# Optimization experiments

Hardware: AMD Instinct MI355X
Metric: run time of the kernel (lower is better)

## Reference

```python
import jax, jax.numpy as jnp
import numpy as np

C = 256
G = 32  # GroupNorm groups
EPS = 1e-6


def setup_inputs() -> dict:
    key = jax.random.key(0)
    ks = jax.random.split(key, 11)
    B, H, W = 4, 64, 64
    scale = 0.02
    return {
        "x": jax.random.normal(ks[0], (B, C, H, W), dtype=jnp.float32),
        "gn_scale": jnp.ones((C,), jnp.float32),
        "gn_bias": jnp.zeros((C,), jnp.float32),
        "wq": jax.random.normal(ks[1], (C, C), jnp.float32) * scale,
        "bq": jnp.zeros((C,), jnp.float32),
        "wk": jax.random.normal(ks[2], (C, C), jnp.float32) * scale,
        "bk": jnp.zeros((C,), jnp.float32),
        "wv": jax.random.normal(ks[3], (C, C), jnp.float32) * scale,
        "bv": jnp.zeros((C,), jnp.float32),
        "wp": jax.random.normal(ks[4], (C, C), jnp.float32) * scale,
        "bp": jnp.zeros((C,), jnp.float32),
    }


def _group_norm(x, scale, bias):
    b, c, h, w = x.shape
    xr = x.reshape(b, G, c // G, h, w)
    mu = jnp.mean(xr, axis=(2, 3, 4), keepdims=True)
    var = jnp.var(xr, axis=(2, 3, 4), keepdims=True)
    xn = ((xr - mu) * jax.lax.rsqrt(var + EPS)).reshape(b, c, h, w)
    return xn * scale[None, :, None, None] + bias[None, :, None, None]


def _conv1x1(x, w, bch):
    # 1x1 conv == channel-mixing matmul; w is (out_ch, in_ch)
    return jnp.einsum('bchw,dc->bdhw', x, w) + bch[None, :, None, None]


def reference(x, gn_scale, gn_bias, wq, bq, wk, bk, wv, bv, wp, bp):
    b, c, h, w = x.shape
    hn = _group_norm(x, gn_scale, gn_bias)
    q = _conv1x1(hn, wq, bq).reshape(b, c, h * w)  # (b,c,N)
    k = _conv1x1(hn, wk, bk).reshape(b, c, h * w)
    v = _conv1x1(hn, wv, bv).reshape(b, c, h * w)
    # attn[b,i,j] = softmax_j( q_i . k_j / sqrt(c) )
    attn = jax.nn.softmax(jnp.einsum('bci,bcj->bij', q, k) * (c ** -0.5), axis=-1)
    A = jnp.einsum('bcj,bij->bci', v, attn).reshape(b, c, h, w)
    return x + _conv1x1(A, wp, bp)
```

## Files before the change

### kernel.cpp

```cpp
#include <hip/hip_runtime.h>
#include <stdint.h>

#define Bn 4
#define Cn 256
#define Gn 32
#define Nn 4096
#define CGn 8

typedef unsigned short u16;
typedef __attribute__((ext_vector_type(8))) short short8;
typedef __attribute__((ext_vector_type(4))) short short4v;
typedef __attribute__((ext_vector_type(4))) float f32x4;
typedef __attribute__((ext_vector_type(16))) float f32x16;

__device__ __forceinline__ u16 f2bf(float x) {
  uint32_t u = __float_as_uint(x);
  u += 0x7fffu + ((u >> 16) & 1u);
  return (u16)(u >> 16);
}
__device__ __forceinline__ float b2f(u16 v) {
  return __uint_as_float(((uint32_t)v) << 16);
}

__device__ __forceinline__ void gl_lds16(const void* g, void* l) {
  __builtin_amdgcn_global_load_lds(
      (__attribute__((address_space(1))) void*)(uintptr_t)g,
      (__attribute__((address_space(3))) void*)(uintptr_t)l, 16, 0, 0);
}

__device__ __forceinline__ int sw512(int row, int cb) { return row * 512 + ((cb ^ (row & 7)) * 16); }

__global__ void k_cs(const float* __restrict__ wq, const float* __restrict__ wk,
                     const float* __restrict__ wv, const float* __restrict__ wp,
                     const float* __restrict__ bq, const float* __restrict__ bk,
                     const float* __restrict__ bv, const float* __restrict__ x,
                     u16* __restrict__ wqkv, u16* __restrict__ wpb,
                     float* __restrict__ bqkv, float* __restrict__ stats) {
  if (blockIdx.x < 256) {
    const float s = 0.09016844005556021f;
    int i = blockIdx.x * 256 + threadIdx.x;
    wqkv[i]          = f2bf(wq[i] * s);
    wqkv[i + 65536]  = f2bf(wk[i]);
    wqkv[i + 131072] = f2bf(wv[i]);
    wpb[i]           = f2bf(wp[i]);
    if (i < 256) { bqkv[i] = bq[i] * s; bqkv[i + 256] = bk[i]; bqkv[i + 512] = bv[i]; }
  } else {
    int blk = blockIdx.x - 256;
    int grp = blk >> 2, part = blk & 3;
    const float4* base = (const float4*)(x + (size_t)grp * (CGn * Nn) + part * 8192);
    float s = 0.f, s2 = 0.f;
    for (int i = threadIdx.x; i < 2048; i += 256) {
      float4 v = base[i];
      s  += v.x + v.y + v.z + v.w;
      s2 += v.x * v.x + v.y * v.y + v.z * v.z + v.w * v.w;
    }
#pragma unroll
    for (int m = 1; m < 64; m <<= 1) { s += __shfl_xor(s, m, 64); s2 += __shfl_xor(s2, m, 64); }
    __shared__ float ps[4], ps2[4];
    int w = threadIdx.x >> 6;
    if ((threadIdx.x & 63) == 0) { ps[w] = s; ps2[w] = s2; }
    __syncthreads();
    if (threadIdx.x == 0) {
      stats[grp * 8 + part * 2]     = ps[0] + ps[1] + ps[2] + ps[3];
      stats[grp * 8 + part * 2 + 1] = ps2[0] + ps2[1] + ps2[2] + ps2[3];
    }
  }
}

__global__ void k_apply(const float* __restrict__ x, const float* __restrict__ stats,
                        const float* __restrict__ gsc, const float* __restrict__ gbi,
                        u16* __restrict__ hnT) {
  __shared__ __align__(16) char smem[32768];
  __shared__ float smu[Gn], srs[Gn];
  int n0 = blockIdx.x * 64;
  int b = blockIdx.y;
  int tid = threadIdx.x;
  if (tid < Gn) {
    float S = 0.f, S2 = 0.f;
#pragma unroll
    for (int p = 0; p < 4; ++p) {
      S  += stats[(b * Gn + tid) * 8 + p * 2];
      S2 += stats[(b * Gn + tid) * 8 + p * 2 + 1];
    }
    const float inv = 1.f / (CGn * Nn);
    float mu = S * inv;
    float var = S2 * inv - mu * mu;
    smu[tid] = mu;
    srs[tid] = rsqrtf(var + 1e-6f);
  }
  __syncthreads();
  int nl = (tid & 15) * 4;
  int cbase = tid >> 4;
  for (int pass = 0; pass < 16; ++pass) {
    int c = pass * 16 + cbase;
    float4 v = *(const float4*)(x + (size_t)b * Cn * Nn + (size_t)c * Nn + n0 + nl);
    int g = c >> 3;
    float sc = gsc[c] * srs[g];
    float bi = gbi[c] - smu[g] * sc;
    float vals[4] = {v.x, v.y, v.z, v.w};
#pragma unroll
    for (int i = 0; i < 4; ++i) {
      int row = nl + i;
      int off = row * 512 + ((((c >> 3) + row) & 31) * 16) + (c & 7) * 2;
      *(u16*)(smem + off) = f2bf(vals[i] * sc + bi);
    }
  }
  __syncthreads();
#pragma unroll
  for (int p = 0; p < 8; ++p) {
    int idx = p * 256 + tid;
    int row = idx >> 5, pc = idx & 31;
    int gc = (pc - row) & 31;
    short8 v8 = *(const short8*)(smem + row * 512 + pc * 16);
    *(short8*)(hnT + ((size_t)b * Nn + n0 + row) * Cn + gc * 8) = v8;
  }
}

__global__ __launch_bounds__(256, 2)
void k_qkv(const u16* __restrict__ wqkv, const float* __restrict__ bqkv,
           const u16* __restrict__ hnT, u16* __restrict__ qT, u16* __restrict__ kT,
           u16* __restrict__ vv) {
  __shared__ __align__(16) char smem[65536];
  int tid = threadIdx.x, lane = tid & 63, w = tid >> 6, quad = lane >> 4, low = lane & 15;
  int n0 = blockIdx.x * 64, d0 = blockIdx.y * 64, b = blockIdx.z;
  {
    int r0 = w * 16;
#pragma unroll
    for (int s = 0; s < 8; ++s) {
      int rs = r0 + s * 2;
      int r = rs + (lane >> 5);
      int cb = (lane & 31) ^ (r & 7);
      gl_lds16(wqkv + (size_t)(d0 + r) * Cn + cb * 8, smem + rs * 512);
      gl_lds16(hnT + ((size_t)b * Nn + n0 + r) * Cn + cb * 8, smem + 32768 + rs * 512);
    }
  }
  asm volatile("s_waitcnt vmcnt(0)" ::: "memory");
  __syncthreads();
  f32x4 acc[4] = {{0.f,0.f,0.f,0.f},{0.f,0.f,0.f,0.f},{0.f,0.f,0.f,0.f},{0.f,0.f,0.f,0.f}};
#pragma unroll
  for (int kk = 0; kk < 8; ++kk) {
    short8 af = *(const short8*)(smem + sw512(w * 16 + low, kk * 4 + quad));
#pragma unroll
    for (int t = 0; t < 4; ++t) {
      short8 bf = *(const short8*)(smem + 32768 + sw512(t * 16 + low, kk * 4 + quad));
      acc[t] = __builtin_amdgcn_mfma_f32_16x16x32_bf16(af, bf, acc[t], 0, 0, 0);
    }
  }
  int which = d0 >> 8;
  float bias[4];
#pragma unroll
  for (int r = 0; r < 4; ++r) bias[r] = bqkv[d0 + w * 16 + quad * 4 + r];
  __syncthreads();
  if (which == 2) {
#pragma unroll
    for (int t = 0; t < 4; ++t)
#pragma unroll
      for (int r = 0; r < 4; ++r) {
        int row = w * 16 + quad * 4 + r;
        int col = t * 16 + low;
        int off = row * 128 + ((((col >> 3) ^ ((row >> 1) & 7)) & 7) * 16) + (col & 7) * 2;
        *(u16*)(smem + off) = f2bf(acc[t][r] + bias[r]);
      }
  } else {
#pragma unroll
    for (int t = 0; t < 4; ++t)
#pragma unroll
      for (int r = 0; r < 4; ++r) {
        int row = t * 16 + low;
        int col = w * 16 + quad * 4 + r;
        int off = row * 128 + ((((col >> 3) ^ ((row >> 1) & 7)) & 7) * 16) + (col & 7) * 2;
        *(u16*)(smem + off) = f2bf(acc[t][r] + bias[r]);
      }
  }
  __syncthreads();
  int dl0 = d0 & 255;
#pragma unroll
  for (int p = 0; p < 2; ++p) {
    int idx = p * 256 + tid;
    int row = idx >> 3, pc = idx & 7;
    int cb = pc ^ ((row >> 1) & 7);
    short8 v8 = *(const short8*)(smem + row * 128 + pc * 16);
    if (which == 2)
      *(short8*)(vv + (size_t)b * Cn * Nn + (size_t)(dl0 + row) * Nn + n0 + cb * 8) = v8;
    else {
      u16* dst = (which == 0 ? qT : kT) + (size_t)b * Nn * Cn;
      *(short8*)(dst + (size_t)(n0 + row) * Cn + dl0 + cb * 8) = v8;
    }
  }
}

__device__ __forceinline__ void flash_stage(char* smem, int bsel, const u16* kTb,
                                            const u16* vb, int j0, int w, int lo,
                                            int kr, int vr, int vp) {
  char* ksb = smem + bsel * 32768;
  char* vsb = ksb + 16384;
#pragma unroll
  for (int s = 0; s < 4; ++s) {
    int j = kr + s * 2;
    int gc = (lo - j) & 31;
    gl_lds16(kTb + (size_t)(j0 + j) * Cn + gc * 8, ksb + (w * 8 + s * 2) * 512);
  }
#pragma unroll
  for (int s = 0; s < 4; ++s) {
    int c = vr + s * 16;
    int gc = (vp - c) & 3;
    gl_lds16(vb + (size_t)c * Nn + j0 + gc * 8, vsb + (w * 64 + s * 16) * 64);
  }
}

__global__ __launch_bounds__(256, 2)
void k_flash(const u16* __restrict__ qT, const u16* __restrict__ kT,
             const u16* __restrict__ vv, u16* __restrict__ Op0,
             u16* __restrict__ Op1, u16* __restrict__ Op2, u16* __restrict__ Op3,
             float* __restrict__ lrow) {
  __shared__ __align__(16) char smem[65536];
  const int tid = threadIdx.x, lane = tid & 63, w = tid >> 6;
  const int lo = lane & 31, hi = lane >> 5;
  const int i0 = blockIdx.x * 128;
  const int b = blockIdx.y, jh = blockIdx.z;
  const u16* qTb = qT + (size_t)b * Nn * Cn;
  const u16* kTb = kT + (size_t)b * Nn * Cn;
  const u16* vb  = vv + (size_t)b * Cn * Nn;
  const int u7 = lo + hi;
  const int kr = w * 8 + hi;
  const int vr = w * 64 + (lane >> 2);
  const int vp = lane & 3;

  flash_stage(smem, 0, kTb, vb, jh * 1024, w, lo, kr, vr, vp);

  short8 qf[16];
  {
    const u16* qrow = qTb + (size_t)(i0 + w * 32 + lo) * Cn + hi * 8;
#pragma unroll
    for (int ks = 0; ks < 16; ++ks) qf[ks] = *(const short8*)(qrow + ks * 16);
  }
  f32x16 Oa[8];
#pragma unroll
  for (int ct = 0; ct < 8; ++ct)
#pragma unroll
    for (int e = 0; e < 16; ++e) Oa[ct][e] = 0.f;
  float l_ = 0.f;

  for (int jt = 0; jt < 32; ++jt) {
    if (jt < 31) {
      flash_stage(smem, (jt + 1) & 1, kTb, vb, jh * 1024 + (jt + 1) * 32, w, lo, kr, vr, vp);
      asm volatile("s_waitcnt vmcnt(8)" ::: "memory");
    } else {
      asm volatile("s_waitcnt vmcnt(0)" ::: "memory");
    }
    asm volatile("s_barrier" ::: "memory");
    const char* ksb = smem + (jt & 1) * 32768;
    const char* vsb = ksb + 16384;

    f32x16 S0;
#pragma unroll
    for (int e = 0; e < 16; ++e) S0[e] = 0.f;
#pragma unroll
    for (int ks = 0; ks < 16; ++ks) {
      int ch = (ks * 2 + u7) & 31;
      short8 a0 = *(const short8*)(ksb + lo * 512 + ch * 16);
      S0 = __builtin_amdgcn_mfma_f32_32x32x16_bf16(a0, qf[ks], S0, 0, 0, 0);
    }
    uint32_t Pp[8];
#pragma unroll
    for (int g = 0; g < 8; ++g) {
      float p0 = __builtin_amdgcn_exp2f(S0[2 * g]);
      float p1 = __builtin_amdgcn_exp2f(S0[2 * g + 1]);
      l_ += p0 + p1;
      Pp[g] = ((uint32_t)f2bf(p1) << 16) | f2bf(p0);
    }
#pragma unroll
    for (int kst = 0; kst < 2; ++kst) {
      uint32_t a0 = Pp[4 * kst], a1 = Pp[4 * kst + 1];
      uint32_t b0 = Pp[4 * kst + 2], b1 = Pp[4 * kst + 3];
      uint32_t s0 = hi ? a0 : b0, s1 = hi ? a1 : b1;
      uint32_t r0 = (uint32_t)__shfl_xor((int)s0, 32, 64);
      uint32_t r1 = (uint32_t)__shfl_xor((int)s1, 32, 64);
      union { uint32_t u[4]; short8 s8; } pu;
      pu.u[0] = hi ? r0 : a0;
      pu.u[1] = hi ? r1 : a1;
      pu.u[2] = hi ? b0 : r0;
      pu.u[3] = hi ? b1 : r1;
      int ch = (kst * 2 + u7) & 3;
#pragma unroll
      for (int ct = 0; ct < 8; ++ct) {
        short8 vf = *(const short8*)(vsb + (ct * 32 + lo) * 64 + ch * 16);
        Oa[ct] = __builtin_amdgcn_mfma_f32_32x32x16_bf16(vf, pu.s8, Oa[ct], 0, 0, 0);
      }
    }
    asm volatile("s_barrier" ::: "memory");
  }

  l_ += __shfl_xor(l_, 32, 64);
  if (hi == 0)
    lrow[(size_t)jh * (Bn * Nn) + (size_t)b * Nn + i0 + w * 32 + lo] = l_;
  float invl = __builtin_amdgcn_rcpf(l_);
  __syncthreads();
#pragma unroll
  for (int ct = 0; ct < 8; ++ct)
#pragma unroll
    for (int g = 0; g < 4; ++g) {
      short4v pk;
#pragma unroll
      for (int r = 0; r < 4; ++r) pk[r] = (short)f2bf(Oa[ct][g * 4 + r] * invl);
      int chv = (ct * 4 + g + lo) & 31;
      *(short4v*)(smem + w * 16384 + lo * 512 + chv * 16 + hi * 8) = pk;
    }
  __syncthreads();
  u16* Opj = (jh == 0) ? Op0 : (jh == 1) ? Op1 : (jh == 2) ? Op2 : Op3;
  u16* Ob = Opj + ((size_t)b * Nn + i0 + w * 32) * (size_t)Cn;
#pragma unroll
  for (int s = 0; s < 16; ++s) {
    int rr = s * 2 + hi;
    short8 v8 = *(const short8*)(smem + w * 16384 + rr * 512 + lo * 16);
    int gc = (lo - rr) & 31;
    *(short8*)(Ob + (size_t)rr * Cn + gc * 8) = v8;
  }
}

__global__ __launch_bounds__(256, 2)
void k_proj(const u16* __restrict__ wpb, const float* __restrict__ bp,
            const u16* __restrict__ O0, const u16* __restrict__ O1,
            const u16* __restrict__ O2, const u16* __restrict__ O3,
            const float* __restrict__ lrow, const float* __restrict__ x,
            float* __restrict__ out) {
  __shared__ __align__(16) char smem[65536];
  int tid = threadIdx.x, lane = tid & 63, w = tid >> 6, quad = lane >> 4, low = lane & 15;
  int n0 = blockIdx.x * 64, d0 = blockIdx.y * 64, b = blockIdx.z;
  {
    int r0 = w * 16;
#pragma unroll
    for (int s = 0; s < 8; ++s) {
      int rs = r0 + s * 2;
      int r = rs + (lane >> 5);
      int cb = (lane & 31) ^ (r & 7);
      gl_lds16(wpb + (size_t)(d0 + r) * Cn + cb * 8, smem + rs * 512);
    }
#pragma unroll
    for (int s = 0; s < 8; ++s) {
      int rs = r0 + s * 2 + (lane >> 5);
      int cb = lane & 31;
      size_t rg = (size_t)b * Nn + n0 + rs;
      float L = lrow[rg] + lrow[(size_t)Bn * Nn + rg] +
                lrow[2 * (size_t)Bn * Nn + rg] + lrow[3 * (size_t)Bn * Nn + rg];
      float inv = __builtin_amdgcn_rcpf(L);
      size_t off = rg * Cn + cb * 8;
      short8 a0 = *(const short8*)(O0 + off);
      short8 a1 = *(const short8*)(O1 + off);
      short8 a2 = *(const short8*)(O2 + off);
      short8 a3 = *(const short8*)(O3 + off);
      short8 o;
#pragma unroll
      for (int e = 0; e < 8; ++e)
        o[e] = (short)f2bf((b2f((u16)a0[e]) + b2f((u16)a1[e]) +
                            b2f((u16)a2[e]) + b2f((u16)a3[e])) * inv);
      *(short8*)(smem + 32768 + rs * 512 + ((cb ^ (rs & 7)) * 16)) = o;
    }
  }
  asm volatile("s_waitcnt vmcnt(0)" ::: "memory");
  __syncthreads();
  f32x4 acc[4] = {{0.f,0.f,0.f,0.f},{0.f,0.f,0.f,0.f},{0.f,0.f,0.f,0.f},{0.f,0.f,0.f,0.f}};
#pragma unroll
  for (int kk = 0; kk < 8; ++kk) {
    short8 af = *(const short8*)(smem + sw512(w * 16 + low, kk * 4 + quad));
#pragma unroll
    for (int t = 0; t < 4; ++t) {
      short8 bf = *(const short8*)(smem + 32768 + sw512(t * 16 + low, kk * 4 + quad));
      acc[t] = __builtin_amdgcn_mfma_f32_16x16x32_bf16(af, bf, acc[t], 0, 0, 0);
    }
  }
  int dloc = d0 + w * 16 + quad * 4;
#pragma unroll
  for (int t = 0; t < 4; ++t)
#pragma unroll
    for (int r = 0; r < 4; ++r) {
      size_t idx = (size_t)b * Cn * Nn + (size_t)(dloc + r) * Nn + n0 + t * 16 + low;
      out[idx] = x[idx] + acc[t][r] + bp[dloc + r];
    }
}

extern "C" void kernel_launch(void* const* d_in, const int* in_sizes, int n_in,
                              void* d_out, int out_size, void* d_ws, size_t ws_size,
                              hipStream_t stream) {
  const float* x   = (const float*)d_in[0];
  const float* gsc = (const float*)d_in[1];
  const float* gbi = (const float*)d_in[2];
  const float* wq  = (const float*)d_in[3];
  const float* bq  = (const float*)d_in[4];
  const float* wk  = (const float*)d_in[5];
  const float* bk  = (const float*)d_in[6];
  const float* wv  = (const float*)d_in[7];
  const float* bv  = (const float*)d_in[8];
  const float* wp  = (const float*)d_in[9];
  const float* bp  = (const float*)d_in[10];
  float* out = (float*)d_out;

  char* ws = (char*)d_ws;
  u16*   wqkv  = (u16*)(ws + 0);
  u16*   wpb   = (u16*)(ws + 393216);
  float* bqkv  = (float*)(ws + 524288);
  float* stats = (float*)(ws + 527360);
  float* lrow  = (float*)(ws + 532480);
  u16*   hnT   = (u16*)(ws + 1048576);
  u16*   qT    = (u16*)(ws + 9437184);
  u16*   kT    = (u16*)(ws + 17825792);
  u16*   vv    = (u16*)(ws + 26214400);
  u16*   Op1   = (u16*)(ws + 34603008);
  u16*   Op2   = (u16*)(ws + 42991616);
  u16*   Op3   = (u16*)(ws + 51380224);

  k_cs<<<768, 256, 0, stream>>>(wq, wk, wv, wp, bq, bk, bv, x, wqkv, wpb, bqkv, stats);
  k_apply<<<dim3(64, 4), 256, 0, stream>>>(x, stats, gsc, gbi, hnT);
  k_qkv<<<dim3(64, 12, 4), 256, 0, stream>>>(wqkv, bqkv, hnT, qT, kT, vv);
  k_flash<<<dim3(32, 4, 4), 256, 0, stream>>>(qT, kT, vv, hnT , Op1, Op2, Op3, lrow);
  k_proj<<<dim3(64, 4, 4), 256, 0, stream>>>(wpb, bp, hnT, Op1, Op2, Op3, lrow, x, out);
}
```

Before: 205.8 us.

## Split split-K combine into separate kernel and rework V LDS swizzle

Moves the four-way split-K combine and normalization out of k_proj into a new k_comb kernel that writes a combined bf16 O buffer (reusing qT storage). k_proj then loads that buffer directly into LDS with async global-to-LDS copies, like the weight tile. The aim is to stop each of the four d-blocks from redundantly combining the same O rows. The V tile swizzle in k_flash also gains an extra (c>>2) term to cut LDS bank conflicts. The cost is an extra kernel launch and an extra full read and write of O.

```diff
diff --git a/kernel.cpp b/kernel.cpp
--- a/kernel.cpp
+++ b/kernel.cpp
@@ -203,7 +203,7 @@
 #pragma unroll
   for (int s = 0; s < 4; ++s) {
     int c = vr + s * 16;
-    int gc = (vp - c) & 3;
+    int gc = (vp - c - (c >> 2)) & 3;
     gl_lds16(vb + (size_t)c * Nn + j0 + gc * 8, vsb + (w * 64 + s * 16) * 64);
   }
 }
@@ -222,6 +222,7 @@
   const u16* kTb = kT + (size_t)b * Nn * Cn;
   const u16* vb  = vv + (size_t)b * Cn * Nn;
   const int u7 = lo + hi;
+  const int u9 = lo + hi + (lo >> 2);
   const int kr = w * 8 + hi;
   const int vr = w * 64 + (lane >> 2);
   const int vp = lane & 3;
@@ -281,7 +282,7 @@
       pu.u[1] = hi ? r1 : a1;
       pu.u[2] = hi ? b0 : r0;
       pu.u[3] = hi ? b1 : r1;
-      int ch = (kst * 2 + u7) & 3;
+      int ch = (kst * 2 + u9) & 3;
 #pragma unroll
       for (int ct = 0; ct < 8; ++ct) {
         short8 vf = *(const short8*)(vsb + (ct * 32 + lo) * 64 + ch * 16);
@@ -318,11 +319,29 @@
   }
 }
 
+__global__ void k_comb(const u16* __restrict__ O0, const u16* __restrict__ O1,
+                       const u16* __restrict__ O2, const u16* __restrict__ O3,
+                       const float* __restrict__ lrow, u16* __restrict__ OT) {
+  int gid = blockIdx.x * 256 + threadIdx.x;
+  int row = gid >> 6;
+  int c4 = (gid & 63) << 2;
+  float L = lrow[row] + lrow[Bn * Nn + row] + lrow[2 * Bn * Nn + row] + lrow[3 * Bn * Nn + row];
+  float inv = __builtin_amdgcn_rcpf(L);
+  size_t base = (size_t)row * Cn + c4;
+  short4v a0 = *(const short4v*)(O0 + base);
+  short4v a1 = *(const short4v*)(O1 + base);
+  short4v a2 = *(const short4v*)(O2 + base);
+  short4v a3 = *(const short4v*)(O3 + base);
+  short4v o;
+#pragma unroll
+  for (int i = 0; i < 4; ++i)
+    o[i] = (short)f2bf((b2f((u16)a0[i]) + b2f((u16)a1[i]) + b2f((u16)a2[i]) + b2f((u16)a3[i])) * inv);
+  *(short4v*)(OT + base) = o;
+}
+
 __global__ __launch_bounds__(256, 2)
 void k_proj(const u16* __restrict__ wpb, const float* __restrict__ bp,
-            const u16* __restrict__ O0, const u16* __restrict__ O1,
-            const u16* __restrict__ O2, const u16* __restrict__ O3,
-            const float* __restrict__ lrow, const float* __restrict__ x,
+            const u16* __restrict__ OT, const float* __restrict__ x,
             float* __restrict__ out) {
   __shared__ __align__(16) char smem[65536];
   int tid = threadIdx.x, lane = tid & 63, w = tid >> 6, quad = lane >> 4, low = lane & 15;
@@ -335,26 +354,7 @@
       int r = rs + (lane >> 5);
       int cb = (lane & 31) ^ (r & 7);
       gl_lds16(wpb + (size_t)(d0 + r) * Cn + cb * 8, smem + rs * 512);
-    }
-#pragma unroll
-    for (int s = 0; s < 8; ++s) {
-      int rs = r0 + s * 2 + (lane >> 5);
-      int cb = lane & 31;
-      size_t rg = (size_t)b * Nn + n0 + rs;
-      float L = lrow[rg] + lrow[(size_t)Bn * Nn + rg] +
-                lrow[2 * (size_t)Bn * Nn + rg] + lrow[3 * (size_t)Bn * Nn + rg];
-      float inv = __builtin_amdgcn_rcpf(L);
-      size_t off = rg * Cn + cb * 8;
-      short8 a0 = *(const short8*)(O0 + off);
-      short8 a1 = *(const short8*)(O1 + off);
-      short8 a2 = *(const short8*)(O2 + off);
-      short8 a3 = *(const short8*)(O3 + off);
-      short8 o;
-#pragma unroll
-      for (int e = 0; e < 8; ++e)
-        o[e] = (short)f2bf((b2f((u16)a0[e]) + b2f((u16)a1[e]) +
-                            b2f((u16)a2[e]) + b2f((u16)a3[e])) * inv);
-      *(short8*)(smem + 32768 + rs * 512 + ((cb ^ (rs & 7)) * 16)) = o;
+      gl_lds16(OT + ((size_t)b * Nn + n0 + r) * Cn + cb * 8, smem + 32768 + rs * 512);
     }
   }
   asm volatile("s_waitcnt vmcnt(0)" ::: "memory");
@@ -413,5 +413,6 @@
   k_apply<<<dim3(64, 4), 256, 0, stream>>>(x, stats, gsc, gbi, hnT);
   k_qkv<<<dim3(64, 12, 4), 256, 0, stream>>>(wqkv, bqkv, hnT, qT, kT, vv);
   k_flash<<<dim3(32, 4, 4), 256, 0, stream>>>(qT, kT, vv, hnT , Op1, Op2, Op3, lrow);
-  k_proj<<<dim3(64, 4, 4), 256, 0, stream>>>(wpb, bp, hnT, Op1, Op2, Op3, lrow, x, out);
-}
+  k_comb<<<4096, 256, 0, stream>>>(hnT, Op1, Op2, Op3, lrow, qT );
+  k_proj<<<dim3(64, 4, 4), 256, 0, stream>>>(wpb, bp, qT , x, out);
+}
```

Result: no change. 202.5 us (-1.6%).
